# Performance work log

Hardware: AMD Instinct MI355X
Metric: run time of the kernel (lower is better)

## Reference

```python
import jax, jax.numpy as jnp
import numpy as np

D = 1024            # BIGNET_DIM
GS = 16             # group_size
NG = D * D // GS    # groups per layer = 65536
N_LAYERS = 18       # 6 blocks * 3 linears
LORA_LAYERS = {0: 0, 6: 1, 12: 2}  # linear index -> lora slot (first linear of blocks 0,2,4)
RANK = 32
BATCH = 16384
EPS = 1e-5


def setup_inputs() -> dict:
    key = jax.random.key(0)
    ks = jax.random.split(key, 6)
    x = jax.random.normal(ks[0], (BATCH, D), dtype=jnp.float32)
    w_q = jax.random.randint(ks[1], (N_LAYERS, NG, GS), 0, 16, dtype=jnp.int32)
    w_norm = jax.random.uniform(ks[2], (N_LAYERS, NG, 1), dtype=jnp.float32)
    bias = jax.random.normal(ks[3], (N_LAYERS, D), dtype=jnp.float32) * 0.02
    lora_a = jax.random.normal(ks[4], (3, RANK, D), dtype=jnp.float32) * (1.0 / np.sqrt(D))
    lora_b = jax.random.normal(ks[5], (3, D, RANK), dtype=jnp.float32) * 0.02
    ln_w = jnp.ones((6, D), dtype=jnp.float32)
    ln_b = jnp.zeros((6, D), dtype=jnp.float32)
    return {"x": x, "w_q": w_q, "w_norm": w_norm, "bias": bias,
            "lora_a": lora_a, "lora_b": lora_b, "ln_w": ln_w, "ln_b": ln_b}


def _dequant(q, n):
    # block_dequantize_4bit: codes in [0,15] -> [-norm, +norm] per group
    return ((q.astype(jnp.float32) / 15.0) * 2.0 - 1.0) * n  # [NG, GS]


def reference(x, w_q, w_norm, bias, lora_a, lora_b, ln_w, ln_b):
    h = x
    for blk in range(6):
        for pos in range(3):
            l = blk * 3 + pos
            W = _dequant(w_q[l], w_norm[l]).reshape(D, D)  # [out, in]
            out = h @ W.T + bias[l]
            if l in LORA_LAYERS:
                i = LORA_LAYERS[l]
                out = out + (h @ lora_a[i].T) @ lora_b[i].T
            if pos < 2:
                out = jax.nn.relu(out)
            h = out
        mu = jnp.mean(h, axis=-1, keepdims=True)
        var = jnp.mean(jnp.square(h - mu), axis=-1, keepdims=True)
        h = (h - mu) * jax.lax.rsqrt(var + EPS) * ln_w[blk] + ln_b[blk]
    return h
```

## Files before the change

### kernel.cpp

```cpp
#include <hip/hip_runtime.h>
#include <cstdint>
#include <cstddef>


typedef short  bf16x8 __attribute__((ext_vector_type(8)));
typedef float  f32x4  __attribute__((ext_vector_type(4)));

__device__ __forceinline__ unsigned short f2bf(float f) {
  unsigned int u = __builtin_bit_cast(unsigned int, f);
  u += 0x7FFFu + ((u >> 16) & 1u);
  return (unsigned short)(u >> 16);
}

__device__ __forceinline__ void async_copy16(void* lds, const void* g) {
  __builtin_amdgcn_global_load_lds(
      (const __attribute__((address_space(1))) void*)(uintptr_t)(g),
      (__attribute__((address_space(3))) void*)(unsigned int)(uintptr_t)(lds),
      16, 0, 0);
}

__global__ __launch_bounds__(256) void lora_kernel(
    const float* __restrict__ lora_a,
    const float* __restrict__ lora_b,
    float* __restrict__ LA) {
  const int slot = blockIdx.y;
  const int o0   = blockIdx.x * 4;
  const int t    = threadIdx.x;
  const float* A = lora_a + slot * 32768 + t * 4;
  const float* B = lora_b + slot * 32768 + o0 * 32;

  float acc[4][4];
#pragma unroll
  for (int k = 0; k < 4; ++k)
#pragma unroll
    for (int j = 0; j < 4; ++j) acc[k][j] = 0.f;

#pragma unroll 8
  for (int r = 0; r < 32; ++r) {
    const float4 a4 = *(const float4*)(A + r * 1024);
#pragma unroll
    for (int k = 0; k < 4; ++k) {
      const float br = B[k * 32 + r];
      acc[k][0] = fmaf(br, a4.x, acc[k][0]);
      acc[k][1] = fmaf(br, a4.y, acc[k][1]);
      acc[k][2] = fmaf(br, a4.z, acc[k][2]);
      acc[k][3] = fmaf(br, a4.w, acc[k][3]);
    }
  }
#pragma unroll
  for (int k = 0; k < 4; ++k) {
    float4 o = make_float4(acc[k][0], acc[k][1], acc[k][2], acc[k][3]);
    *(float4*)(LA + (size_t)slot * 1048576 + (size_t)(o0 + k) * 1024 + t * 4) = o;
  }
}

__global__ __launch_bounds__(256) void dequant_kernel(
    const int* __restrict__ wq, const float* __restrict__ wn,
    const float* __restrict__ LA,
    unsigned short* __restrict__ Wbf) {
  const int l   = blockIdx.y;
  const int t   = threadIdx.x;
  const int blk = blockIdx.x;
  const long base = (long)l * 1048576;
  const float s = 2.0f / 15.0f;

  const int slot = (l == 0) ? 0 : (l == 6) ? 1 : (l == 12) ? 2 : -1;

  int4  q[4];
  float nrm[4];
  float4 c4[4];
#pragma unroll
  for (int k = 0; k < 4; ++k) {
    const int i4 = blk * 1024 + k * 256 + t;
    q[k]   = *(const int4*)(wq + base + (long)i4 * 4);
    nrm[k] = wn[l * 65536 + (i4 >> 2)];
  }
  if (slot >= 0) {
    const float* LAp = LA + (size_t)slot * 1048576;
#pragma unroll
    for (int k = 0; k < 4; ++k) {
      const int i4 = blk * 1024 + k * 256 + t;
      c4[k] = *(const float4*)(LAp + (size_t)i4 * 4);
    }
  }

  float v[4][4];
#pragma unroll
  for (int k = 0; k < 4; ++k) {
    v[k][0] = ((float)q[k].x * s - 1.0f) * nrm[k];
    v[k][1] = ((float)q[k].y * s - 1.0f) * nrm[k];
    v[k][2] = ((float)q[k].z * s - 1.0f) * nrm[k];
    v[k][3] = ((float)q[k].w * s - 1.0f) * nrm[k];
  }
  if (slot >= 0) {
#pragma unroll
    for (int k = 0; k < 4; ++k) {
      v[k][0] += c4[k].x; v[k][1] += c4[k].y;
      v[k][2] += c4[k].z; v[k][3] += c4[k].w;
    }
  }

#pragma unroll
  for (int k = 0; k < 4; ++k) {
    unsigned short u[4] = {f2bf(v[k][0]), f2bf(v[k][1]),
                           f2bf(v[k][2]), f2bf(v[k][3])};
    const long e0 = base + ((long)blk * 1024 + k * 256 + t) * 4;
    *(uint2*)(Wbf + e0) = *(uint2*)u;
  }
}

__global__ __launch_bounds__(256) void cvt_bf16_kernel(
    const float* __restrict__ in, unsigned short* __restrict__ out) {
  const long b0 = (long)blockIdx.x * 4096 + threadIdx.x * 4;
  float4 v[4];
#pragma unroll
  for (int k = 0; k < 4; ++k) v[k] = *(const float4*)(in + b0 + k * 1024);
#pragma unroll
  for (int k = 0; k < 4; ++k) {
    unsigned short u[4] = {f2bf(v[k].x), f2bf(v[k].y), f2bf(v[k].z), f2bf(v[k].w)};
    *(ushort4*)(out + b0 + k * 1024) = *(ushort4*)u;
  }
}

template <int MODE, int SWAP>
__global__ __launch_bounds__(256, 4) void gemm_kernel(
    const unsigned short* __restrict__ H,
    const unsigned short* __restrict__ W,
    const float* __restrict__ bias,
    unsigned short* __restrict__ outb,
    float* __restrict__ outf) {
  constexpr int K = 1024;
  constexpr int NN = 1024;

  __shared__ uint4 ldsq[2048];
  char* base = (char*)ldsq;

  const int tid = threadIdx.x;
  const int w   = tid >> 6;
  const int ln  = tid & 63;
  const int b   = blockIdx.x;
  const int m0  = ((b & 7) * 16 + (b >> 6)) * 128;
  const int n0  = ((b >> 3) & 7) * 128;

  const int gc = (ln & 7) ^ (ln >> 3);
  const unsigned short* gA = H + (size_t)(m0 + w * 32 + (ln >> 3)) * K + gc * 8;
  const unsigned short* gB = W + (size_t)(n0 + w * 32 + (ln >> 3)) * K + gc * 8;
  char* ldsA = base + w * 4096;
  char* ldsB = base + 16384 + w * 4096;

  const int quad = ln >> 4;
  const int lrow = ln & 15;
  const int sw   = lrow & 7;
  const int c0   = ((quad)     ^ sw) * 16;
  const int c1   = ((quad + 4) ^ sw) * 16;
  const int wm   = (w >> 1) * 64;
  const int wn   = (w & 1) * 64;
  const char* fragA = base + (wm + lrow) * 128;
  const char* fragB = base + 16384 + (wn + lrow) * 128;

  f32x4 acc[4][4];
#pragma unroll
  for (int i = 0; i < 4; ++i)
#pragma unroll
    for (int j = 0; j < 4; ++j) acc[i][j] = (f32x4){0.f, 0.f, 0.f, 0.f};

  for (int kt = 0; kt < 16; ++kt) {
    const unsigned short* pA = gA + kt * 64;
    const unsigned short* pB = gB + kt * 64;
#pragma unroll
    for (int i = 0; i < 4; ++i) {
      async_copy16(ldsA + i * 1024, pA + (size_t)i * 8 * K);
      async_copy16(ldsB + i * 1024, pB + (size_t)i * 8 * K);
    }
    __syncthreads();
#pragma unroll
    for (int kk = 0; kk < 2; ++kk) {
      const int co = kk ? c1 : c0;
      bf16x8 af[4], bg[4];
#pragma unroll
      for (int mt = 0; mt < 4; ++mt)
        af[mt] = *(const bf16x8*)(fragA + mt * 2048 + co);
#pragma unroll
      for (int nt = 0; nt < 4; ++nt)
        bg[nt] = *(const bf16x8*)(fragB + nt * 2048 + co);
#pragma unroll
      for (int mt = 0; mt < 4; ++mt)
#pragma unroll
        for (int nt = 0; nt < 4; ++nt) {
          if (SWAP) {
            acc[mt][nt] = __builtin_amdgcn_mfma_f32_16x16x32_bf16(
                bg[nt], af[mt], acc[mt][nt], 0, 0, 0);
          } else {
            acc[mt][nt] = __builtin_amdgcn_mfma_f32_16x16x32_bf16(
                af[mt], bg[nt], acc[mt][nt], 0, 0, 0);
          }
        }
    }
    __syncthreads();
  }

  if (SWAP) {
#pragma unroll
    for (int mt = 0; mt < 4; ++mt) {
      const size_t row = (size_t)(m0 + wm + mt * 16 + lrow);
#pragma unroll
      for (int nt = 0; nt < 4; ++nt) {
        const int nb = n0 + wn + nt * 16 + quad * 4;
        const float4 bs = *(const float4*)(bias + nb);
        const f32x4 v = acc[mt][nt];
        float o0 = v[0] + bs.x, o1 = v[1] + bs.y;
        float o2 = v[2] + bs.z, o3 = v[3] + bs.w;
        if (MODE == 0) {
          o0 = fmaxf(o0, 0.0f); o1 = fmaxf(o1, 0.0f);
          o2 = fmaxf(o2, 0.0f); o3 = fmaxf(o3, 0.0f);
        }
        if (MODE == 1) {
          *(float4*)(outf + row * NN + nb) = make_float4(o0, o1, o2, o3);
        } else {
          unsigned short u[4] = {f2bf(o0), f2bf(o1), f2bf(o2), f2bf(o3)};
          *(uint2*)(outb + row * NN + nb) = *(uint2*)u;
        }
      }
    }
  } else {
#pragma unroll
    for (int nt = 0; nt < 4; ++nt) {
      const int n = n0 + wn + nt * 16 + lrow;
      const float bs = bias[n];
#pragma unroll
      for (int mt = 0; mt < 4; ++mt) {
        const int mb = m0 + wm + mt * 16 + quad * 4;
        f32x4 v = acc[mt][nt];
#pragma unroll
        for (int r = 0; r < 4; ++r) {
          float o = v[r] + bs;
          if (MODE == 0) o = fmaxf(o, 0.0f);
          if (MODE == 1) {
            outf[(size_t)(mb + r) * NN + n] = o;
          } else {
            outb[(size_t)(mb + r) * NN + n] = f2bf(o);
          }
        }
      }
    }
  }
}

__global__ __launch_bounds__(256) void ln_kernel(
    const float* __restrict__ in, const float* __restrict__ lnw,
    const float* __restrict__ lnb, unsigned short* __restrict__ outb,
    float* __restrict__ outf, int wbf, int wf32) {
  const int wv = threadIdx.x >> 6;
  const int ln = threadIdx.x & 63;
  const int row = blockIdx.x * 4 + wv;
  const float* p = in + (size_t)row * 1024;

  float4 v[4];
  float s = 0.f, q = 0.f;
#pragma unroll
  for (int c = 0; c < 4; ++c) {
    v[c] = *(const float4*)(p + c * 256 + ln * 4);
    s += v[c].x + v[c].y + v[c].z + v[c].w;
    q += v[c].x * v[c].x + v[c].y * v[c].y + v[c].z * v[c].z + v[c].w * v[c].w;
  }
#pragma unroll
  for (int off = 32; off; off >>= 1) {
    s += __shfl_xor(s, off);
    q += __shfl_xor(q, off);
  }
  const float mu  = s * (1.0f / 1024.0f);
  const float var = q * (1.0f / 1024.0f) - mu * mu;
  const float rs  = rsqrtf(var + 1e-5f);

#pragma unroll
  for (int c = 0; c < 4; ++c) {
    const int col = c * 256 + ln * 4;
    const float4 w4 = *(const float4*)(lnw + col);
    const float4 b4 = *(const float4*)(lnb + col);
    const float y0 = (v[c].x - mu) * rs * w4.x + b4.x;
    const float y1 = (v[c].y - mu) * rs * w4.y + b4.y;
    const float y2 = (v[c].z - mu) * rs * w4.z + b4.z;
    const float y3 = (v[c].w - mu) * rs * w4.w + b4.w;
    if (wbf) {
      unsigned short u[4] = {f2bf(y0), f2bf(y1), f2bf(y2), f2bf(y3)};
      *(ushort4*)(outb + (size_t)row * 1024 + col) = *(ushort4*)u;
    }
    if (wf32) {
      float4 y = make_float4(y0, y1, y2, y3);
      *(float4*)(outf + (size_t)row * 1024 + col) = y;
    }
  }
}

__global__ __launch_bounds__(256) void ln_bf16_kernel(
    const unsigned short* __restrict__ in, const float* __restrict__ lnw,
    const float* __restrict__ lnb, unsigned short* __restrict__ outb) {
  const int wv = threadIdx.x >> 6;
  const int ln = threadIdx.x & 63;
  const int row = blockIdx.x * 4 + wv;
  const unsigned short* p = in + (size_t)row * 1024 + ln * 16;

  const uint4 r0 = *(const uint4*)(p);
  const uint4 r1 = *(const uint4*)(p + 8);
  const unsigned ru[8] = {r0.x, r0.y, r0.z, r0.w, r1.x, r1.y, r1.z, r1.w};

  float f[16];
#pragma unroll
  for (int i = 0; i < 8; ++i) {
    f[2 * i]     = __builtin_bit_cast(float, ru[i] << 16);
    f[2 * i + 1] = __builtin_bit_cast(float, ru[i] & 0xffff0000u);
  }

  float s = 0.f, q = 0.f;
#pragma unroll
  for (int i = 0; i < 16; ++i) { s += f[i]; q += f[i] * f[i]; }
#pragma unroll
  for (int off = 32; off; off >>= 1) {
    s += __shfl_xor(s, off);
    q += __shfl_xor(q, off);
  }
  const float mu  = s * (1.0f / 1024.0f);
  const float var = q * (1.0f / 1024.0f) - mu * mu;
  const float rs  = rsqrtf(var + 1e-5f);

  const float* wp = lnw + ln * 16;
  const float* bp = lnb + ln * 16;
  unsigned o[8];
#pragma unroll
  for (int i = 0; i < 8; ++i) {
    const float y0 = (f[2 * i]     - mu) * rs * wp[2 * i]     + bp[2 * i];
    const float y1 = (f[2 * i + 1] - mu) * rs * wp[2 * i + 1] + bp[2 * i + 1];
    o[i] = (unsigned)f2bf(y0) | ((unsigned)f2bf(y1) << 16);
  }
  unsigned short* dst = outb + (size_t)row * 1024 + ln * 16;
  *(uint4*)(dst)     = make_uint4(o[0], o[1], o[2], o[3]);
  *(uint4*)(dst + 8) = make_uint4(o[4], o[5], o[6], o[7]);
}

extern "C" void kernel_launch(void* const* d_in, const int* in_sizes, int n_in,
                              void* d_out, int out_size, void* d_ws, size_t ws_size,
                              hipStream_t stream) {
  const float* x    = (const float*)d_in[0];
  const int*   wq   = (const int*)d_in[1];
  const float* wn   = (const float*)d_in[2];
  const float* bias = (const float*)d_in[3];
  const float* la   = (const float*)d_in[4];
  const float* lb   = (const float*)d_in[5];
  const float* lnw  = (const float*)d_in[6];
  const float* lnb  = (const float*)d_in[7];
  float* out = (float*)d_out;

  char* ws = (char*)d_ws;
  unsigned short* Wbf = (unsigned short*)ws;
  unsigned short* hA  = (unsigned short*)(ws + 37748736);
  unsigned short* hB  = (unsigned short*)(ws + 37748736 + 33554432);
  float* LA = (float*)hB;

  lora_kernel<<<dim3(256, 3), 256, 0, stream>>>(la, lb, LA);
  dequant_kernel<<<dim3(256, 18), 256, 0, stream>>>(wq, wn, LA, Wbf);
  cvt_bf16_kernel<<<4096, 256, 0, stream>>>(x, hA);

  for (int blk = 0; blk < 6; ++blk) {
    const int l = blk * 3;
    if ((blk & 1) == 0) {
      gemm_kernel<0, 1><<<1024, 256, 0, stream>>>(
          hA, Wbf + (size_t)l * 1048576, bias + l * 1024, hB, nullptr);
      gemm_kernel<0, 1><<<1024, 256, 0, stream>>>(
          hB, Wbf + (size_t)(l + 1) * 1048576, bias + (l + 1) * 1024, hA, nullptr);
      gemm_kernel<2, 1><<<1024, 256, 0, stream>>>(
          hA, Wbf + (size_t)(l + 2) * 1048576, bias + (l + 2) * 1024, hB, nullptr);
      ln_bf16_kernel<<<4096, 256, 0, stream>>>(
          hB, lnw + blk * 1024, lnb + blk * 1024, hA);
    } else if (blk < 5) {
      gemm_kernel<0, 0><<<1024, 256, 0, stream>>>(
          hA, Wbf + (size_t)l * 1048576, bias + l * 1024, hB, nullptr);
      gemm_kernel<0, 0><<<1024, 256, 0, stream>>>(
          hB, Wbf + (size_t)(l + 1) * 1048576, bias + (l + 1) * 1024, hA, nullptr);
      gemm_kernel<2, 0><<<1024, 256, 0, stream>>>(
          hA, Wbf + (size_t)(l + 2) * 1048576, bias + (l + 2) * 1024, hB, nullptr);
      ln_bf16_kernel<<<4096, 256, 0, stream>>>(
          hB, lnw + blk * 1024, lnb + blk * 1024, hA);
    } else {
      gemm_kernel<0, 0><<<1024, 256, 0, stream>>>(
          hA, Wbf + (size_t)l * 1048576, bias + l * 1024, hB, nullptr);
      gemm_kernel<0, 0><<<1024, 256, 0, stream>>>(
          hB, Wbf + (size_t)(l + 1) * 1048576, bias + (l + 1) * 1024, hA, nullptr);
      gemm_kernel<1, 0><<<1024, 256, 0, stream>>>(
          hA, Wbf + (size_t)(l + 2) * 1048576, bias + (l + 2) * 1024, nullptr, out);
      ln_kernel<<<4096, 256, 0, stream>>>(
          out, lnw + blk * 1024, lnb + blk * 1024, nullptr, out, 0, 1);
    }
  }
}
```

Before: 978.2 us.

## Use register-direct GEMM for even blocks and vectorized epilogue everywhere

Adds a GEMM variant that loads MFMA fragments directly from global memory into registers, skipping LDS staging and barriers, and uses it for blocks 0, 2 and 4. The LDS GEMM is simplified to always use the swapped operand order, so every layer gets the row-contiguous float4/uint2 epilogue instead of scalar strided stores. The register path drops LDS sharing between waves, so each tile is fetched from cache twice with no prefetch overlap.

```diff
diff --git a/kernel.cpp b/kernel.cpp
--- a/kernel.cpp
+++ b/kernel.cpp
@@ -122,7 +122,80 @@
   }
 }
 
-template <int MODE, int SWAP>
+template <int MODE>
+__global__ __launch_bounds__(256, 4) void gemm_reg_kernel(
+    const unsigned short* __restrict__ H,
+    const unsigned short* __restrict__ W,
+    const float* __restrict__ bias,
+    unsigned short* __restrict__ outb,
+    float* __restrict__ outf) {
+  constexpr int NN = 1024;
+  const int tid = threadIdx.x;
+  const int w   = tid >> 6;
+  const int ln  = tid & 63;
+  const int b   = blockIdx.x;
+  const int m0  = ((b & 7) * 16 + (b >> 6)) * 128;
+  const int n0  = ((b >> 3) & 7) * 128;
+
+  const int quad = ln >> 4;
+  const int lrow = ln & 15;
+  const int wm   = (w >> 1) * 64;
+  const int wn   = (w & 1) * 64;
+
+  const unsigned short* pA = H + (size_t)(m0 + wm + lrow) * 1024 + quad * 8;
+  const unsigned short* pB = W + (size_t)(n0 + wn + lrow) * 1024 + quad * 8;
+
+  f32x4 acc[4][4];
+#pragma unroll
+  for (int i = 0; i < 4; ++i)
+#pragma unroll
+    for (int j = 0; j < 4; ++j) acc[i][j] = (f32x4){0.f, 0.f, 0.f, 0.f};
+
+  for (int kt = 0; kt < 16; ++kt) {
+#pragma unroll
+    for (int kk = 0; kk < 2; ++kk) {
+      const int ko = kt * 64 + kk * 32;
+      bf16x8 af[4], bg[4];
+#pragma unroll
+      for (int mt = 0; mt < 4; ++mt)
+        af[mt] = *(const bf16x8*)(pA + (size_t)mt * 16384 + ko);
+#pragma unroll
+      for (int nt = 0; nt < 4; ++nt)
+        bg[nt] = *(const bf16x8*)(pB + (size_t)nt * 16384 + ko);
+#pragma unroll
+      for (int mt = 0; mt < 4; ++mt)
+#pragma unroll
+        for (int nt = 0; nt < 4; ++nt)
+          acc[mt][nt] = __builtin_amdgcn_mfma_f32_16x16x32_bf16(
+              bg[nt], af[mt], acc[mt][nt], 0, 0, 0);
+    }
+  }
+
+#pragma unroll
+  for (int mt = 0; mt < 4; ++mt) {
+    const size_t row = (size_t)(m0 + wm + mt * 16 + lrow);
+#pragma unroll
+    for (int nt = 0; nt < 4; ++nt) {
+      const int nb = n0 + wn + nt * 16 + quad * 4;
+      const float4 bs = *(const float4*)(bias + nb);
+      const f32x4 v = acc[mt][nt];
+      float o0 = v[0] + bs.x, o1 = v[1] + bs.y;
+      float o2 = v[2] + bs.z, o3 = v[3] + bs.w;
+      if (MODE == 0) {
+        o0 = fmaxf(o0, 0.0f); o1 = fmaxf(o1, 0.0f);
+        o2 = fmaxf(o2, 0.0f); o3 = fmaxf(o3, 0.0f);
+      }
+      if (MODE == 1) {
+        *(float4*)(outf + row * NN + nb) = make_float4(o0, o1, o2, o3);
+      } else {
+        unsigned short u[4] = {f2bf(o0), f2bf(o1), f2bf(o2), f2bf(o3)};
+        *(uint2*)(outb + row * NN + nb) = *(uint2*)u;
+      }
+    }
+  }
+}
+
+template <int MODE>
 __global__ __launch_bounds__(256, 4) void gemm_kernel(
     const unsigned short* __restrict__ H,
     const unsigned short* __restrict__ W,
@@ -186,61 +259,32 @@
 #pragma unroll
       for (int mt = 0; mt < 4; ++mt)
 #pragma unroll
-        for (int nt = 0; nt < 4; ++nt) {
-          if (SWAP) {
-            acc[mt][nt] = __builtin_amdgcn_mfma_f32_16x16x32_bf16(
-                bg[nt], af[mt], acc[mt][nt], 0, 0, 0);
-          } else {
-            acc[mt][nt] = __builtin_amdgcn_mfma_f32_16x16x32_bf16(
-                af[mt], bg[nt], acc[mt][nt], 0, 0, 0);
-          }
-        }
+        for (int nt = 0; nt < 4; ++nt)
+          acc[mt][nt] = __builtin_amdgcn_mfma_f32_16x16x32_bf16(
+              bg[nt], af[mt], acc[mt][nt], 0, 0, 0);
     }
     __syncthreads();
   }
 
-  if (SWAP) {
-#pragma unroll
-    for (int mt = 0; mt < 4; ++mt) {
-      const size_t row = (size_t)(m0 + wm + mt * 16 + lrow);
-#pragma unroll
-      for (int nt = 0; nt < 4; ++nt) {
-        const int nb = n0 + wn + nt * 16 + quad * 4;
-        const float4 bs = *(const float4*)(bias + nb);
-        const f32x4 v = acc[mt][nt];
-        float o0 = v[0] + bs.x, o1 = v[1] + bs.y;
-        float o2 = v[2] + bs.z, o3 = v[3] + bs.w;
-        if (MODE == 0) {
-          o0 = fmaxf(o0, 0.0f); o1 = fmaxf(o1, 0.0f);
-          o2 = fmaxf(o2, 0.0f); o3 = fmaxf(o3, 0.0f);
-        }
-        if (MODE == 1) {
-          *(float4*)(outf + row * NN + nb) = make_float4(o0, o1, o2, o3);
-        } else {
-          unsigned short u[4] = {f2bf(o0), f2bf(o1), f2bf(o2), f2bf(o3)};
-          *(uint2*)(outb + row * NN + nb) = *(uint2*)u;
-        }
+#pragma unroll
+  for (int mt = 0; mt < 4; ++mt) {
+    const size_t row = (size_t)(m0 + wm + mt * 16 + lrow);
+#pragma unroll
+    for (int nt = 0; nt < 4; ++nt) {
+      const int nb = n0 + wn + nt * 16 + quad * 4;
+      const float4 bs = *(const float4*)(bias + nb);
+      const f32x4 v = acc[mt][nt];
+      float o0 = v[0] + bs.x, o1 = v[1] + bs.y;
+      float o2 = v[2] + bs.z, o3 = v[3] + bs.w;
+      if (MODE == 0) {
+        o0 = fmaxf(o0, 0.0f); o1 = fmaxf(o1, 0.0f);
+        o2 = fmaxf(o2, 0.0f); o3 = fmaxf(o3, 0.0f);
       }
-    }
-  } else {
-#pragma unroll
-    for (int nt = 0; nt < 4; ++nt) {
-      const int n = n0 + wn + nt * 16 + lrow;
-      const float bs = bias[n];
-#pragma unroll
-      for (int mt = 0; mt < 4; ++mt) {
-        const int mb = m0 + wm + mt * 16 + quad * 4;
-        f32x4 v = acc[mt][nt];
-#pragma unroll
-        for (int r = 0; r < 4; ++r) {
-          float o = v[r] + bs;
-          if (MODE == 0) o = fmaxf(o, 0.0f);
-          if (MODE == 1) {
-            outf[(size_t)(mb + r) * NN + n] = o;
-          } else {
-            outb[(size_t)(mb + r) * NN + n] = f2bf(o);
-          }
-        }
+      if (MODE == 1) {
+        *(float4*)(outf + row * NN + nb) = make_float4(o0, o1, o2, o3);
+      } else {
+        unsigned short u[4] = {f2bf(o0), f2bf(o1), f2bf(o2), f2bf(o3)};
+        *(uint2*)(outb + row * NN + nb) = *(uint2*)u;
       }
     }
   }
@@ -363,29 +407,29 @@
   for (int blk = 0; blk < 6; ++blk) {
     const int l = blk * 3;
     if ((blk & 1) == 0) {
-      gemm_kernel<0, 1><<<1024, 256, 0, stream>>>(
+      gemm_reg_kernel<0><<<1024, 256, 0, stream>>>(
           hA, Wbf + (size_t)l * 1048576, bias + l * 1024, hB, nullptr);
-      gemm_kernel<0, 1><<<1024, 256, 0, stream>>>(
+      gemm_reg_kernel<0><<<1024, 256, 0, stream>>>(
           hB, Wbf + (size_t)(l + 1) * 1048576, bias + (l + 1) * 1024, hA, nullptr);
-      gemm_kernel<2, 1><<<1024, 256, 0, stream>>>(
+      gemm_reg_kernel<2><<<1024, 256, 0, stream>>>(
           hA, Wbf + (size_t)(l + 2) * 1048576, bias + (l + 2) * 1024, hB, nullptr);
       ln_bf16_kernel<<<4096, 256, 0, stream>>>(
           hB, lnw + blk * 1024, lnb + blk * 1024, hA);
     } else if (blk < 5) {
-      gemm_kernel<0, 0><<<1024, 256, 0, stream>>>(
+      gemm_kernel<0><<<1024, 256, 0, stream>>>(
           hA, Wbf + (size_t)l * 1048576, bias + l * 1024, hB, nullptr);
-      gemm_kernel<0, 0><<<1024, 256, 0, stream>>>(
+      gemm_kernel<0><<<1024, 256, 0, stream>>>(
           hB, Wbf + (size_t)(l + 1) * 1048576, bias + (l + 1) * 1024, hA, nullptr);
-      gemm_kernel<2, 0><<<1024, 256, 0, stream>>>(
+      gemm_kernel<2><<<1024, 256, 0, stream>>>(
           hA, Wbf + (size_t)(l + 2) * 1048576, bias + (l + 2) * 1024, hB, nullptr);
       ln_bf16_kernel<<<4096, 256, 0, stream>>>(
           hB, lnw + blk * 1024, lnb + blk * 1024, hA);
     } else {
-      gemm_kernel<0, 0><<<1024, 256, 0, stream>>>(
+      gemm_kernel<0><<<1024, 256, 0, stream>>>(
           hA, Wbf + (size_t)l * 1048576, bias + l * 1024, hB, nullptr);
-      gemm_kernel<0, 0><<<1024, 256, 0, stream>>>(
+      gemm_kernel<0><<<1024, 256, 0, stream>>>(
           hB, Wbf + (size_t)(l + 1) * 1048576, bias + (l + 1) * 1024, hA, nullptr);
-      gemm_kernel<1, 0><<<1024, 256, 0, stream>>>(
+      gemm_kernel<1><<<1024, 256, 0, stream>>>(
           hA, Wbf + (size_t)(l + 2) * 1048576, bias + (l + 2) * 1024, nullptr, out);
       ln_kernel<<<4096, 256, 0, stream>>>(
           out, lnw + blk * 1024, lnb + blk * 1024, nullptr, out, 0, 1);
```

Result: slower. 1.755 ms (+79.4%).
